# Performance work log

Measured on AMD Instinct MI355X. Metric: run time of the kernel, lower is better.

The kernel has to match this reference:

```python
import jax, jax.numpy as jnp
import numpy as np
from jax import lax

N, F, V = 16, 5, 4  # batch, frames, nodes-per-frame

def _maxpool3(x):
    # MaxPool2d(kernel=3, stride=3), NCHW
    return lax.reduce_window(x, -jnp.inf, lax.max, (1, 1, 3, 3), (1, 1, 3, 3), 'VALID')

def _conv(x, w, b):
    y = lax.conv_general_dilated(x, w, window_strides=(2, 2), padding='VALID',
                                 dimension_numbers=('NCHW', 'OIHW', 'NCHW'))
    return y + b[None, :, None, None]

def setup_inputs() -> dict:
    key = jax.random.key(0)
    ks = jax.random.split(key, 24)
    s = 0.05
    inp = {
        'nodes':  jax.random.normal(ks[0], (N, F, V, 3, 224, 224), jnp.float32),
        'pos':    jax.random.normal(ks[1], (N, F, V, 6), jnp.float32),
        'attmap': jax.random.uniform(ks[2], (N, F, V, V), jnp.float32),
        'depths': jax.random.normal(ks[3], (N, F, V), jnp.float32),
        # params (linear weights stored [in, out]; y = x @ W + b)
        'conv1_w': jax.random.normal(ks[4], (3, 3, 3, 3), jnp.float32) * s,
        'conv1_b': jax.random.normal(ks[5], (3,), jnp.float32) * s,
        'conv2_w': jax.random.normal(ks[6], (1, 3, 3, 3), jnp.float32) * s,
        'conv2_b': jax.random.normal(ks[7], (1,), jnp.float32) * s,
        'lin_w':   jax.random.normal(ks[8], (36, 6), jnp.float32) * s,
        'lin_b':   jax.random.normal(ks[9], (6,), jnp.float32) * s,
        'wfc_w':   jax.random.normal(ks[10], (24, 1), jnp.float32) * s,
        'wfc_b':   jax.random.normal(ks[11], (1,), jnp.float32) * s,
        'fm_w':    jax.random.normal(ks[12], (6, 6), jnp.float32) * s,
        'fm_b':    jax.random.normal(ks[13], (6,), jnp.float32) * s,
        'lm_w':    jax.random.normal(ks[14], (6, 6), jnp.float32) * s,
        'lm_b':    jax.random.normal(ks[15], (6,), jnp.float32) * s,
        'fc1_w':   jax.random.normal(ks[16], (240, 120), jnp.float32) * s,
        'fc1_b':   jax.random.normal(ks[17], (120,), jnp.float32) * s,
        'fc2_w':   jax.random.normal(ks[18], (120, 60), jnp.float32) * s,
        'fc2_b':   jax.random.normal(ks[19], (60,), jnp.float32) * s,
        'fc3_w':   jax.random.normal(ks[20], (60, 6), jnp.float32) * s,
        'fc3_b':   jax.random.normal(ks[21], (6,), jnp.float32) * s,
    }
    return inp

def reference(nodes, pos, attmap, depths,
              conv1_w, conv1_b, conv2_w, conv2_b, lin_w, lin_b,
              wfc_w, wfc_b, fm_w, fm_b, lm_w, lm_b,
              fc1_w, fc1_b, fc2_w, fc2_b, fc3_w, fc3_b):
    # --- CNN node encoder ---
    x = nodes.reshape(N * F * V, 3, 224, 224)
    h = jax.nn.relu(_maxpool3(_conv(x, conv1_w, conv1_b)))          # [B*,3,37,37]
    h = jax.nn.relu(_maxpool3(_conv(h, conv2_w, conv2_b)))          # [B*,1,6,6]
    feat = h.reshape(N, F, V, 36) @ lin_w + lin_b                    # [N,F,V,6]

    # --- edge weights: sigmoid(W . cat(feat_src, feat_tgt)) ---
    na = jnp.concatenate([feat, pos], axis=-1)                       # [N,F,V,12]
    src = jnp.broadcast_to(na[:, :, :, None, :], (N, F, V, V, 12))   # s along axis 2
    tgt = jnp.broadcast_to(na[:, :, None, :, :], (N, F, V, V, 12))   # t along axis 3
    ef = jnp.concatenate([src, tgt], axis=-1)                        # [N,F,V,V,24]
    link = jax.nn.sigmoid((ef @ wfc_w)[..., 0] + wfc_b[0])           # [N,F,s,t]

    maw = link + attmap                                              # [N,F,s,t]

    # --- attention-weighted message aggregation over source nodes ---
    pm = pos @ fm_w + fm_b                                           # [N,F,V,6]
    agg = jnp.einsum('bfsn,bfsd->bfnd', maw, pm)                     # [N,F,V,6]

    # last-frame message (frame 0 has none)
    prev = jnp.concatenate([jnp.zeros_like(pos[:, :1]), pos[:, :-1]], axis=1)
    lm = prev @ lm_w + lm_b                                          # [N,F,V,6]
    frame_mask = (jnp.arange(F) > 0)[None, :, None, None]
    pos_up = agg + jnp.where(frame_mask, lm, 0.0)

    # --- readout MLP ---
    inp = jnp.concatenate([feat, pos_up], axis=-1).reshape(N, F * V * 12)  # [N,240]
    r = jax.nn.relu(inp @ fc1_w + fc1_b)
    r = jax.nn.relu(r @ fc2_w + fc2_b)
    return r @ fc3_w + fc3_b                                         # [N,6]
```

## Files before the change

kernel.cpp:

```cpp
#include <hip/hip_runtime.h>
#include <math.h>

#define NB 16
#define NF 5
#define NV 4
#define NIMG (NB*NF*NV)
#define IMG_HW 224
#define IMG_CH_STRIDE (224*224)
#define H1_HW 37
#define H1_CH_STRIDE (37*37)

__global__ __launch_bounds__(256) void k1_conv1_pool(
    const float* __restrict__ nodes,
    const float* __restrict__ w,
    const float* __restrict__ bias,
    float* __restrict__ h1)
{
    int tid = blockIdx.x * 256 + threadIdx.x;
    const int TOT = NIMG * H1_HW * H1_HW;
    if (tid >= TOT) return;
    int b   = tid / (H1_HW * H1_HW);
    int rem = tid - b * (H1_HW * H1_HW);
    int py  = rem / H1_HW;
    int px  = rem - py * H1_HW;

    const float* inb = nodes + (size_t)b * 3 * IMG_CH_STRIDE;
    const int r0 = 6 * py, c0 = 6 * px;

    float acc[3][9];
    #pragma unroll
    for (int oc = 0; oc < 3; ++oc)
        #pragma unroll
        for (int p = 0; p < 9; ++p) acc[oc][p] = 0.f;

    #pragma unroll
    for (int ic = 0; ic < 3; ++ic) {
        float patch[7][7];
        const float* ip = inb + ic * IMG_CH_STRIDE + r0 * IMG_HW + c0;
        #pragma unroll
        for (int r = 0; r < 7; ++r)
            #pragma unroll
            for (int c = 0; c < 7; ++c)
                patch[r][c] = ip[r * IMG_HW + c];

        float wv[3][3][3];
        #pragma unroll
        for (int oc = 0; oc < 3; ++oc)
            #pragma unroll
            for (int ky = 0; ky < 3; ++ky)
                #pragma unroll
                for (int kx = 0; kx < 3; ++kx)
                    wv[oc][ky][kx] = w[((oc * 3 + ic) * 3 + ky) * 3 + kx];

        #pragma unroll
        for (int i = 0; i < 3; ++i)
            #pragma unroll
            for (int j = 0; j < 3; ++j) {
                const int p = i * 3 + j;
                #pragma unroll
                for (int ky = 0; ky < 3; ++ky)
                    #pragma unroll
                    for (int kx = 0; kx < 3; ++kx) {
                        float x = patch[2 * i + ky][2 * j + kx];
                        acc[0][p] += wv[0][ky][kx] * x;
                        acc[1][p] += wv[1][ky][kx] * x;
                        acc[2][p] += wv[2][ky][kx] * x;
                    }
            }
    }

    float* outb = h1 + (size_t)b * 3 * H1_CH_STRIDE + py * H1_HW + px;
    #pragma unroll
    for (int oc = 0; oc < 3; ++oc) {
        float m = -INFINITY;
        #pragma unroll
        for (int p = 0; p < 9; ++p) m = fmaxf(m, acc[oc][p]);
        m += bias[oc];
        m = fmaxf(m, 0.f);
        outb[oc * H1_CH_STRIDE] = m;
    }
}

__global__ __launch_bounds__(64) void k2_conv2_pool_lin(
    const float* __restrict__ h1,
    const float* __restrict__ w2,
    const float* __restrict__ b2,
    const float* __restrict__ lin_w,
    const float* __restrict__ lin_b,
    float* __restrict__ feat)
{
    int b = blockIdx.x;
    int t = threadIdx.x;
    __shared__ float s_h2[36];

    if (t < 36) {
        int py = t / 6, px = t - (t / 6) * 6;
        const float* hb = h1 + (size_t)b * 3 * H1_CH_STRIDE;
        float m = -INFINITY;
        #pragma unroll
        for (int i = 0; i < 3; ++i)
            #pragma unroll
            for (int j = 0; j < 3; ++j) {
                int oy = 3 * py + i, ox = 3 * px + j;
                float a = 0.f;
                #pragma unroll
                for (int ic = 0; ic < 3; ++ic)
                    #pragma unroll
                    for (int ky = 0; ky < 3; ++ky)
                        #pragma unroll
                        for (int kx = 0; kx < 3; ++kx)
                            a += w2[(ic * 3 + ky) * 3 + kx] *
                                 hb[ic * H1_CH_STRIDE + (2 * oy + ky) * H1_HW + (2 * ox + kx)];
                m = fmaxf(m, a);
            }
        m += b2[0];
        s_h2[t] = fmaxf(m, 0.f);
    }
    __syncthreads();
    if (t < 6) {
        float a = lin_b[t];
        #pragma unroll
        for (int i = 0; i < 36; ++i) a += s_h2[i] * lin_w[i * 6 + t];
        feat[b * 6 + t] = a;
    }
}

__global__ __launch_bounds__(128) void k3_graph_mlp(
    const float* __restrict__ feat,
    const float* __restrict__ pos,
    const float* __restrict__ attmap,
    const float* __restrict__ wfc_w,
    const float* __restrict__ wfc_b,
    const float* __restrict__ fm_w,
    const float* __restrict__ fm_b,
    const float* __restrict__ lm_w,
    const float* __restrict__ lm_b,
    const float* __restrict__ fc1_w,
    const float* __restrict__ fc1_b,
    const float* __restrict__ fc2_w,
    const float* __restrict__ fc2_b,
    const float* __restrict__ fc3_w,
    const float* __restrict__ fc3_b,
    float* __restrict__ out)
{
    int b = blockIdx.x;
    int t = threadIdx.x;

    __shared__ float s_na[NF][NV][12];
    __shared__ float s_pm[NF][NV][6];
    __shared__ float s_maw[NF][NV][NV];
    __shared__ float s_inp[240];
    __shared__ float s_r1[120];
    __shared__ float s_r2[60];

    if (t < 120) {
        int f = t / 24;
        int v = (t / 6) % 4;
        int d = t % 6;
        float fv = feat[((b * NF + f) * NV + v) * 6 + d];
        float pv = pos[((b * NF + f) * NV + v) * 6 + d];
        s_na[f][v][d]     = fv;
        s_na[f][v][6 + d] = pv;
        s_inp[(f * NV + v) * 12 + d] = fv;
    }
    __syncthreads();

    if (t < 120) {
        int f = t / 24;
        int v = (t / 6) % 4;
        int d = t % 6;
        float a = fm_b[d];
        #pragma unroll
        for (int k = 0; k < 6; ++k) a += s_na[f][v][6 + k] * fm_w[k * 6 + d];
        s_pm[f][v][d] = a;
    }
    if (t < 80) {
        int f = t / 16;
        int s = (t / 4) % 4;
        int tt = t % 4;
        float x = wfc_b[0];
        #pragma unroll
        for (int k = 0; k < 12; ++k)
            x += wfc_w[k] * s_na[f][s][k] + wfc_w[12 + k] * s_na[f][tt][k];
        float sig = 1.f / (1.f + expf(-x));
        s_maw[f][s][tt] = sig + attmap[((b * NF + f) * NV + s) * NV + tt];
    }
    __syncthreads();

    if (t < 120) {
        int f = t / 24;
        int n = (t / 6) % 4;
        int d = t % 6;
        float a = 0.f;
        #pragma unroll
        for (int s = 0; s < 4; ++s) a += s_maw[f][s][n] * s_pm[f][s][d];
        if (f > 0) {
            float l = lm_b[d];
            #pragma unroll
            for (int k = 0; k < 6; ++k) l += s_na[f - 1][n][6 + k] * lm_w[k * 6 + d];
            a += l;
        }
        s_inp[(f * NV + n) * 12 + 6 + d] = a;
    }
    __syncthreads();

    if (t < 120) {
        float a = fc1_b[t];
        for (int i = 0; i < 240; ++i) a += s_inp[i] * fc1_w[i * 120 + t];
        s_r1[t] = fmaxf(a, 0.f);
    }
    __syncthreads();

    if (t < 60) {
        float a = fc2_b[t];
        for (int i = 0; i < 120; ++i) a += s_r1[i] * fc2_w[i * 60 + t];
        s_r2[t] = fmaxf(a, 0.f);
    }
    __syncthreads();

    if (t < 6) {
        float a = fc3_b[t];
        for (int i = 0; i < 60; ++i) a += s_r2[i] * fc3_w[i * 6 + t];
        out[b * 6 + t] = a;
    }
}

extern "C" void kernel_launch(void* const* d_in, const int* in_sizes, int n_in,
                              void* d_out, int out_size, void* d_ws, size_t ws_size,
                              hipStream_t stream) {
    const float* nodes   = (const float*)d_in[0];
    const float* pos     = (const float*)d_in[1];
    const float* attmap  = (const float*)d_in[2];
    const float* conv1_w = (const float*)d_in[4];
    const float* conv1_b = (const float*)d_in[5];
    const float* conv2_w = (const float*)d_in[6];
    const float* conv2_b = (const float*)d_in[7];
    const float* lin_w   = (const float*)d_in[8];
    const float* lin_b   = (const float*)d_in[9];
    const float* wfc_w   = (const float*)d_in[10];
    const float* wfc_b   = (const float*)d_in[11];
    const float* fm_w    = (const float*)d_in[12];
    const float* fm_b    = (const float*)d_in[13];
    const float* lm_w    = (const float*)d_in[14];
    const float* lm_b    = (const float*)d_in[15];
    const float* fc1_w   = (const float*)d_in[16];
    const float* fc1_b   = (const float*)d_in[17];
    const float* fc2_w   = (const float*)d_in[18];
    const float* fc2_b   = (const float*)d_in[19];
    const float* fc3_w   = (const float*)d_in[20];
    const float* fc3_b   = (const float*)d_in[21];

    float* h1      = (float*)d_ws;
    float* feat_ws = h1 + (size_t)NIMG * 3 * H1_CH_STRIDE;

    const int tot1 = NIMG * H1_HW * H1_HW;
    k1_conv1_pool<<<(tot1 + 255) / 256, 256, 0, stream>>>(nodes, conv1_w, conv1_b, h1);
    k2_conv2_pool_lin<<<NIMG, 64, 0, stream>>>(h1, conv2_w, conv2_b, lin_w, lin_b, feat_ws);
    k3_graph_mlp<<<NB, 128, 0, stream>>>(feat_ws, pos, attmap,
                                         wfc_w, wfc_b, fm_w, fm_b, lm_w, lm_b,
                                         fc1_w, fc1_b, fc2_w, fc2_b, fc3_w, fc3_b,
                                         (float*)d_out);
}
```

Measured before the change: 329.5 us.

## Stage conv1 input rows and conv2 images in shared memory via float4 loads

```diff
diff --git a/kernel.cpp b/kernel.cpp
--- a/kernel.cpp
+++ b/kernel.cpp
@@ -9,6 +9,7 @@
 #define IMG_CH_STRIDE (224*224)
 #define H1_HW 37
 #define H1_CH_STRIDE (37*37)
+#define H1_IMG 4108
 
 __global__ __launch_bounds__(256) void k1_conv1_pool(
     const float* __restrict__ nodes,
@@ -16,72 +17,93 @@
     const float* __restrict__ bias,
     float* __restrict__ h1)
 {
-    int tid = blockIdx.x * 256 + threadIdx.x;
-    const int TOT = NIMG * H1_HW * H1_HW;
-    if (tid >= TOT) return;
-    int b   = tid / (H1_HW * H1_HW);
-    int rem = tid - b * (H1_HW * H1_HW);
-    int py  = rem / H1_HW;
-    int px  = rem - py * H1_HW;
-
-    const float* inb = nodes + (size_t)b * 3 * IMG_CH_STRIDE;
-    const int r0 = 6 * py, c0 = 6 * px;
-
-    float acc[3][9];
-    #pragma unroll
-    for (int oc = 0; oc < 3; ++oc)
-        #pragma unroll
-        for (int p = 0; p < 9; ++p) acc[oc][p] = 0.f;
-
-    #pragma unroll
-    for (int ic = 0; ic < 3; ++ic) {
-        float patch[7][7];
-        const float* ip = inb + ic * IMG_CH_STRIDE + r0 * IMG_HW + c0;
-        #pragma unroll
-        for (int r = 0; r < 7; ++r)
-            #pragma unroll
-            for (int c = 0; c < 7; ++c)
-                patch[r][c] = ip[r * IMG_HW + c];
-
-        float wv[3][3][3];
+    const int blk = blockIdx.x;
+    const int img = blk / H1_HW;
+    const int py  = blk - img * H1_HW;
+    const int t   = threadIdx.x;
+
+    __shared__ float s[3 * 7 * 224];
+
+    const float* src = nodes + (size_t)img * 3 * IMG_CH_STRIDE + py * 6 * IMG_HW;
+
+    {
+        const float4* s0 = (const float4*)(src);
+        const float4* s1 = (const float4*)(src + IMG_CH_STRIDE);
+        const float4* s2 = (const float4*)(src + 2 * IMG_CH_STRIDE);
+        float4* d0 = (float4*)s;
+        float4* d1 = (float4*)(s + 1568);
+        float4* d2 = (float4*)(s + 3136);
+        const bool hi = (t < 392 - 256);
+        float4 a0 = s0[t], a1 = s1[t], a2 = s2[t];
+        float4 b0, b1, b2;
+        if (hi) { b0 = s0[t + 256]; b1 = s1[t + 256]; b2 = s2[t + 256]; }
+        d0[t] = a0; d1[t] = a1; d2[t] = a2;
+        if (hi) { d0[t + 256] = b0; d1[t + 256] = b1; d2[t + 256] = b2; }
+    }
+    __syncthreads();
+
+    if (t < H1_HW) {
+        const int px = t;
+        float acc[3][9];
         #pragma unroll
         for (int oc = 0; oc < 3; ++oc)
             #pragma unroll
-            for (int ky = 0; ky < 3; ++ky)
-                #pragma unroll
-                for (int kx = 0; kx < 3; ++kx)
-                    wv[oc][ky][kx] = w[((oc * 3 + ic) * 3 + ky) * 3 + kx];
-
-        #pragma unroll
-        for (int i = 0; i < 3; ++i)
-            #pragma unroll
-            for (int j = 0; j < 3; ++j) {
-                const int p = i * 3 + j;
+            for (int p = 0; p < 9; ++p) acc[oc][p] = 0.f;
+
+        #pragma unroll
+        for (int ic = 0; ic < 3; ++ic) {
+            float wv[3][3][3];
+            #pragma unroll
+            for (int oc = 0; oc < 3; ++oc)
                 #pragma unroll
                 for (int ky = 0; ky < 3; ++ky)
                     #pragma unroll
-                    for (int kx = 0; kx < 3; ++kx) {
-                        float x = patch[2 * i + ky][2 * j + kx];
-                        acc[0][p] += wv[0][ky][kx] * x;
-                        acc[1][p] += wv[1][ky][kx] * x;
-                        acc[2][p] += wv[2][ky][kx] * x;
-                    }
+                    for (int kx = 0; kx < 3; ++kx)
+                        wv[oc][ky][kx] = w[((oc * 3 + ic) * 3 + ky) * 3 + kx];
+
+            float patch[7][8];
+            #pragma unroll
+            for (int r = 0; r < 7; ++r) {
+                const float* row = s + ic * 1568 + r * 224 + 6 * px;
+                #pragma unroll
+                for (int k = 0; k < 4; ++k) {
+                    float2 q = *(const float2*)(row + 2 * k);
+                    patch[r][2 * k]     = q.x;
+                    patch[r][2 * k + 1] = q.y;
+                }
             }
-    }
-
-    float* outb = h1 + (size_t)b * 3 * H1_CH_STRIDE + py * H1_HW + px;
-    #pragma unroll
-    for (int oc = 0; oc < 3; ++oc) {
-        float m = -INFINITY;
-        #pragma unroll
-        for (int p = 0; p < 9; ++p) m = fmaxf(m, acc[oc][p]);
-        m += bias[oc];
-        m = fmaxf(m, 0.f);
-        outb[oc * H1_CH_STRIDE] = m;
+
+            #pragma unroll
+            for (int i = 0; i < 3; ++i)
+                #pragma unroll
+                for (int j = 0; j < 3; ++j) {
+                    const int p = i * 3 + j;
+                    #pragma unroll
+                    for (int ky = 0; ky < 3; ++ky)
+                        #pragma unroll
+                        for (int kx = 0; kx < 3; ++kx) {
+                            float x = patch[2 * i + ky][2 * j + kx];
+                            acc[0][p] += wv[0][ky][kx] * x;
+                            acc[1][p] += wv[1][ky][kx] * x;
+                            acc[2][p] += wv[2][ky][kx] * x;
+                        }
+                }
+        }
+
+        float* outb = h1 + (size_t)img * H1_IMG + py * H1_HW + px;
+        #pragma unroll
+        for (int oc = 0; oc < 3; ++oc) {
+            float m = -INFINITY;
+            #pragma unroll
+            for (int p = 0; p < 9; ++p) m = fmaxf(m, acc[oc][p]);
+            m += bias[oc];
+            m = fmaxf(m, 0.f);
+            outb[oc * H1_CH_STRIDE] = m;
+        }
     }
 }
 
-__global__ __launch_bounds__(64) void k2_conv2_pool_lin(
+__global__ __launch_bounds__(128) void k2_conv2_pool_lin(
     const float* __restrict__ h1,
     const float* __restrict__ w2,
     const float* __restrict__ b2,
@@ -89,19 +111,34 @@
     const float* __restrict__ lin_b,
     float* __restrict__ feat)
 {
-    int b = blockIdx.x;
-    int t = threadIdx.x;
+    const int img = blockIdx.x;
+    const int t   = threadIdx.x;
+    __shared__ float s[H1_IMG];
     __shared__ float s_h2[36];
 
+    {
+        const float4* src = (const float4*)(h1 + (size_t)img * H1_IMG);
+        float4* d = (float4*)s;
+        float4 v[8];
+        #pragma unroll
+        for (int k = 0; k < 8; ++k) v[k] = src[t + 128 * k];
+        const bool hi = (t < 1027 - 1024);
+        float4 v8;
+        if (hi) v8 = src[t + 1024];
+        #pragma unroll
+        for (int k = 0; k < 8; ++k) d[t + 128 * k] = v[k];
+        if (hi) d[t + 1024] = v8;
+    }
+    __syncthreads();
+
     if (t < 36) {
-        int py = t / 6, px = t - (t / 6) * 6;
-        const float* hb = h1 + (size_t)b * 3 * H1_CH_STRIDE;
+        const int py = t / 6, px = t - (t / 6) * 6;
         float m = -INFINITY;
         #pragma unroll
         for (int i = 0; i < 3; ++i)
             #pragma unroll
             for (int j = 0; j < 3; ++j) {
-                int oy = 3 * py + i, ox = 3 * px + j;
+                const int oy = 3 * py + i, ox = 3 * px + j;
                 float a = 0.f;
                 #pragma unroll
                 for (int ic = 0; ic < 3; ++ic)
@@ -110,7 +147,7 @@
                         #pragma unroll
                         for (int kx = 0; kx < 3; ++kx)
                             a += w2[(ic * 3 + ky) * 3 + kx] *
-                                 hb[ic * H1_CH_STRIDE + (2 * oy + ky) * H1_HW + (2 * ox + kx)];
+                                 s[ic * H1_CH_STRIDE + (2 * oy + ky) * H1_HW + (2 * ox + kx)];
                 m = fmaxf(m, a);
             }
         m += b2[0];
@@ -121,7 +158,7 @@
         float a = lin_b[t];
         #pragma unroll
         for (int i = 0; i < 36; ++i) a += s_h2[i] * lin_w[i * 6 + t];
-        feat[b * 6 + t] = a;
+        feat[img * 6 + t] = a;
     }
 }
 
@@ -143,8 +180,8 @@
     const float* __restrict__ fc3_b,
     float* __restrict__ out)
 {
-    int b = blockIdx.x;
-    int t = threadIdx.x;
+    const int b = blockIdx.x;
+    const int t = threadIdx.x;
 
     __shared__ float s_na[NF][NV][12];
     __shared__ float s_pm[NF][NV][6];
@@ -176,14 +213,14 @@
     }
     if (t < 80) {
         int f = t / 16;
-        int s = (t / 4) % 4;
+        int sidx = (t / 4) % 4;
         int tt = t % 4;
         float x = wfc_b[0];
         #pragma unroll
         for (int k = 0; k < 12; ++k)
-            x += wfc_w[k] * s_na[f][s][k] + wfc_w[12 + k] * s_na[f][tt][k];
+            x += wfc_w[k] * s_na[f][sidx][k] + wfc_w[12 + k] * s_na[f][tt][k];
         float sig = 1.f / (1.f + expf(-x));
-        s_maw[f][s][tt] = sig + attmap[((b * NF + f) * NV + s) * NV + tt];
+        s_maw[f][sidx][tt] = sig + attmap[((b * NF + f) * NV + sidx) * NV + tt];
     }
     __syncthreads();
 
@@ -193,7 +230,7 @@
         int d = t % 6;
         float a = 0.f;
         #pragma unroll
-        for (int s = 0; s < 4; ++s) a += s_maw[f][s][n] * s_pm[f][s][d];
+        for (int sidx = 0; sidx < 4; ++sidx) a += s_maw[f][sidx][n] * s_pm[f][sidx][d];
         if (f > 0) {
             float l = lm_b[d];
             #pragma unroll
@@ -206,6 +243,7 @@
 
     if (t < 120) {
         float a = fc1_b[t];
+        #pragma unroll 16
         for (int i = 0; i < 240; ++i) a += s_inp[i] * fc1_w[i * 120 + t];
         s_r1[t] = fmaxf(a, 0.f);
     }
@@ -213,6 +251,7 @@
 
     if (t < 60) {
         float a = fc2_b[t];
+        #pragma unroll 16
         for (int i = 0; i < 120; ++i) a += s_r1[i] * fc2_w[i * 60 + t];
         s_r2[t] = fmaxf(a, 0.f);
     }
@@ -220,6 +259,7 @@
 
     if (t < 6) {
         float a = fc3_b[t];
+        #pragma unroll 12
         for (int i = 0; i < 60; ++i) a += s_r2[i] * fc3_w[i * 6 + t];
         out[b * 6 + t] = a;
     }
@@ -251,11 +291,10 @@
     const float* fc3_b   = (const float*)d_in[21];
 
     float* h1      = (float*)d_ws;
-    float* feat_ws = h1 + (size_t)NIMG * 3 * H1_CH_STRIDE;
-
-    const int tot1 = NIMG * H1_HW * H1_HW;
-    k1_conv1_pool<<<(tot1 + 255) / 256, 256, 0, stream>>>(nodes, conv1_w, conv1_b, h1);
-    k2_conv2_pool_lin<<<NIMG, 64, 0, stream>>>(h1, conv2_w, conv2_b, lin_w, lin_b, feat_ws);
+    float* feat_ws = h1 + (size_t)NIMG * H1_IMG;
+
+    k1_conv1_pool<<<NIMG * H1_HW, 256, 0, stream>>>(nodes, conv1_w, conv1_b, h1);
+    k2_conv2_pool_lin<<<NIMG, 128, 0, stream>>>(h1, conv2_w, conv2_b, lin_w, lin_b, feat_ws);
     k3_graph_mlp<<<NB, 128, 0, stream>>>(feat_ws, pos, attmap,
                                          wfc_w, wfc_b, fm_w, fm_b, lm_w, lm_b,
                                          fc1_w, fc1_b, fc2_w, fc2_b, fc3_w, fc3_b,
```

After: 328.0 us. About the same (-0.5%).
